# Performance work log

Hardware: AMD Instinct MI355X
Metric: run time of the kernel (lower is better)

## Reference

```python
import jax, jax.numpy as jnp
import numpy as np

N_NODES = 100_000
N_EDGES = 3_200_000
NUM_FEATURES = 128
HIDDEN = 128
NUM_CLASSES = 10
LAYERS = 3
NUM_GRAPHS = 256
EPS = 1e-5


def setup_inputs() -> dict:
    key = jax.random.key(0)
    ks = jax.random.split(key, 12)
    s = 0.05
    x = jax.random.normal(ks[0], (N_NODES, NUM_FEATURES), jnp.float32)
    edge_index = jax.random.randint(ks[1], (2, N_EDGES), 0, N_NODES, dtype=jnp.int32)
    batch = jnp.sort(jax.random.randint(ks[2], (N_NODES,), 0, NUM_GRAPHS, dtype=jnp.int32))
    lin1_W = jax.random.normal(ks[3], (NUM_FEATURES, HIDDEN), jnp.float32) * s
    lin1_b = jnp.zeros((HIDDEN,), jnp.float32)
    conv_W = jax.random.normal(ks[4], (LAYERS, HIDDEN, HIDDEN), jnp.float32) * s
    conv_b = jnp.zeros((LAYERS, HIDDEN), jnp.float32)
    mlp_W1 = jax.random.normal(ks[5], (HIDDEN, HIDDEN), jnp.float32) * s
    mlp_b1 = jnp.zeros((HIDDEN,), jnp.float32)
    mlp_W2 = jax.random.normal(ks[6], (HIDDEN, NUM_CLASSES), jnp.float32) * s
    mlp_b2 = jnp.zeros((NUM_CLASSES,), jnp.float32)
    return {
        'x': x, 'edge_index': edge_index, 'batch': batch,
        'lin1_W': lin1_W, 'lin1_b': lin1_b,
        'conv_W': conv_W, 'conv_b': conv_b,
        'mlp_W1': mlp_W1, 'mlp_b1': mlp_b1,
        'mlp_W2': mlp_W2, 'mlp_b2': mlp_b2,
    }


def reference(x, edge_index, batch, lin1_W, lin1_b, conv_W, conv_b,
              mlp_W1, mlp_b1, mlp_W2, mlp_b2):
    N = x.shape[0]
    # GCN with self-loops, all-ones edge_weight, symmetric normalization.
    loop = jnp.arange(N, dtype=edge_index.dtype)
    src = jnp.concatenate([edge_index[0], loop])
    dst = jnp.concatenate([edge_index[1], loop])
    ew = jnp.ones(src.shape[0], x.dtype)
    deg = jax.ops.segment_sum(ew, dst, num_segments=N)
    dinv = jnp.where(deg > 0, jax.lax.rsqrt(deg), 0.0)
    norm = dinv[src] * dinv[dst]  # [E+N]

    h = jax.nn.relu(x @ lin1_W + lin1_b)  # dropout is identity at eval
    for i in range(conv_W.shape[0]):
        hw = h @ conv_W[i]                       # [N,H]
        msg = hw[src] * norm[:, None]            # [E+N,H] gather
        h = jax.ops.segment_sum(msg, dst, num_segments=N) + conv_b[i]
        h = jax.nn.relu(h)
        # full-tensor LayerNorm (normalized_shape == x.size(), no affine)
        mu = jnp.mean(h)
        var = jnp.mean(jnp.square(h - mu))
        h = (h - mu) * jax.lax.rsqrt(var + EPS)

    # global mean pooling over graphs
    cnt = jax.ops.segment_sum(jnp.ones((N,), x.dtype), batch, num_segments=NUM_GRAPHS)
    pooled = jax.ops.segment_sum(h, batch, num_segments=NUM_GRAPHS) / jnp.maximum(cnt, 1.0)[:, None]

    g = jax.nn.relu(pooled @ mlp_W1 + mlp_b1)
    scores = g @ mlp_W2 + mlp_b2
    return jax.nn.log_softmax(scores, axis=-1)
```

## Files before the change

kernel.cpp:

```cpp
#include <hip/hip_runtime.h>
#include <math.h>

#define NN 100000
#define HH 128
#define NCLS 10
#define NGRAPH 256
#define EPSLN 1e-5f
#define NB 196
#define NBLK 256

typedef __attribute__((ext_vector_type(8))) short short8;
typedef __attribute__((ext_vector_type(4))) float f32x4;

static __device__ __forceinline__ unsigned short f2bf(float f){
  unsigned u = __float_as_uint(f);
  u = u + 0x7fffu + ((u >> 16) & 1u);
  return (unsigned short)(u >> 16);
}
static __device__ __forceinline__ float bf2f(unsigned short h){
  return __uint_as_float(((unsigned)h) << 16);
}

__global__ __launch_bounds__(1024) void bucket_hist(
    const int* __restrict__ dst, int E,
    int* __restrict__ gbucket, int* __restrict__ blkbase)
{
  __shared__ int lh[NB];
  int tid = threadIdx.x;
  for (int i = tid; i < NB; i += 1024) lh[i] = 0;
  __syncthreads();
  int per = (E + gridDim.x - 1) / gridDim.x;
  int s = blockIdx.x * per, e = min(E, s + per);
  for (int j = s + tid; j < e; j += 1024)
    atomicAdd(&lh[dst[j] >> 9], 1);
  __syncthreads();
  for (int i = tid; i < NB; i += 1024)
    blkbase[blockIdx.x * NB + i] = atomicAdd(&gbucket[i], lh[i]);
}

__global__ void bucket_scan(const int* __restrict__ gbucket,
                            int* __restrict__ bucket_base, int E,
                            int* __restrict__ row_ptr, int N,
                            float* __restrict__ params, float* __restrict__ stats)
{
  if (threadIdx.x == 0 && blockIdx.x == 0){
    int run = 0;
    for (int b = 0; b < NB; b++){ bucket_base[b] = run; run += gbucket[b]; }
    bucket_base[NB] = run;
    row_ptr[N] = E;
    params[0] = 0.f;
    params[1] = 1.f;
    for (int i = 0; i < 6; i++) stats[i] = 0.f;
  }
}

__global__ __launch_bounds__(1024) void bucket_scatter(
    const int* __restrict__ src, const int* __restrict__ dst, int E,
    const int* __restrict__ bucket_base, const int* __restrict__ blkbase,
    unsigned* __restrict__ ebuf)
{
  __shared__ int lcur[NB];
  int tid = threadIdx.x;
  for (int i = tid; i < NB; i += 1024)
    lcur[i] = bucket_base[i] + blkbase[blockIdx.x * NB + i];
  __syncthreads();
  int per = (E + gridDim.x - 1) / gridDim.x;
  int s = blockIdx.x * per, e = min(E, s + per);
  for (int j = s + tid; j < e; j += 1024){
    int d = dst[j];
    int p = atomicAdd(&lcur[d >> 9], 1);
    ebuf[p] = (((unsigned)(d & 511)) << 23) | (unsigned)src[j];
  }
}

__global__ __launch_bounds__(1024) void bucket_fill(
    const unsigned* __restrict__ ebuf,
    const int* __restrict__ bucket_base, int N,
    int* __restrict__ row_ptr, float* __restrict__ dinv,
    int* __restrict__ csr)
{
  __shared__ int ldeg[512];
  __shared__ int lscan[512];
  __shared__ int lcur[512];
  int b = blockIdx.x, tid = threadIdx.x;
  int node0 = b << 9;
  int nn = min(512, N - node0);
  for (int i = tid; i < 512; i += 1024) ldeg[i] = 0;
  __syncthreads();
  int s = bucket_base[b], e = bucket_base[b + 1];
  for (int j = s + tid; j < e; j += 1024)
    atomicAdd(&ldeg[ebuf[j] >> 23], 1);
  __syncthreads();
  if (tid < 512) lscan[tid] = ldeg[tid];
  __syncthreads();
  for (int off = 1; off < 512; off <<= 1){
    int v = (tid < 512 && tid >= off) ? lscan[tid - off] : 0;
    __syncthreads();
    if (tid < 512) lscan[tid] += v;
    __syncthreads();
  }
  if (tid < nn){
    int rp = s + lscan[tid] - ldeg[tid];
    row_ptr[node0 + tid] = rp;
    lcur[tid] = rp;
    dinv[node0 + tid] = rsqrtf((float)(ldeg[tid] + 1));
  }
  __syncthreads();
  for (int j = s + tid; j < e; j += 1024){
    unsigned pk = ebuf[j];
    int p = atomicAdd(&lcur[pk >> 23], 1);
    csr[p] = (int)(pk & 0x7fffffu);
  }
}

__global__ void colsum_kernel(const float* __restrict__ W, float* __restrict__ cs){
  const float* w = W + blockIdx.x*HH*HH;
  float s = 0.f;
  for (int k = 0; k < HH; k++) s += w[k*HH + threadIdx.x];
  cs[blockIdx.x*HH + threadIdx.x] = s;
}

__global__ __launch_bounds__(256) void prep_weights(
    const float* __restrict__ lin1W, const float* __restrict__ convW,
    unsigned short* __restrict__ WtAll)
{
  int m = blockIdx.x;
  const float* srcW = (m == 0) ? lin1W : convW + (size_t)(m-1)*HH*HH;
  unsigned short* dstW = WtAll + (size_t)m*HH*HH;
  for (int i = threadIdx.x; i < HH*HH; i += 256){
    int k = i >> 7, nn2 = i & 127;
    dstW[nn2*HH + k] = f2bf(srcW[i]);
  }
}

__global__ __launch_bounds__(256) void gemm_mfma(
    const float* __restrict__ A32, const unsigned short* __restrict__ A16,
    const unsigned short* __restrict__ Wt,
    const float* __restrict__ bias, const float* __restrict__ dinv,
    const float* __restrict__ params, const float* __restrict__ colsum,
    unsigned short* __restrict__ out, int n, int mode)
{
  __shared__ unsigned short As[128*128];
  __shared__ unsigned short Ws[128*128];
  int tid = threadIdx.x;
  int rb = blockIdx.x * 128;

  #pragma unroll
  for (int rep = 0; rep < 8; rep++){
    int idx = rep*256 + tid;
    int r = idx >> 4, j = idx & 15;
    uint4 v = *(const uint4*)&Wt[r*HH + j*8];
    *(uint4*)&Ws[r*128 + ((j ^ (r & 7)) << 3)] = v;
  }
  if (mode == 1){
    #pragma unroll
    for (int rep = 0; rep < 8; rep++){
      int idx = rep*256 + tid;
      int r = idx >> 4, j = idx & 15;
      int row = rb + r;
      uint4 v = make_uint4(0,0,0,0);
      if (row < n) v = *(const uint4*)&A16[(size_t)row*HH + j*8];
      *(uint4*)&As[r*128 + ((j ^ (r & 7)) << 3)] = v;
    }
  } else {
    #pragma unroll
    for (int rep = 0; rep < 16; rep++){
      int idx = rep*256 + tid;
      int r = idx >> 5, j4 = idx & 31;
      int row = rb + r;
      float4 v = make_float4(0,0,0,0);
      if (row < n) v = *(const float4*)&A32[(size_t)row*HH + j4*4];
      uint2 pk;
      pk.x = (unsigned)f2bf(v.x) | ((unsigned)f2bf(v.y) << 16);
      pk.y = (unsigned)f2bf(v.z) | ((unsigned)f2bf(v.w) << 16);
      int uidx = r*128 + ((((j4 >> 1) ^ (r & 7)) << 3)) + (j4 & 1)*4;
      *(uint2*)&As[uidx] = pk;
    }
  }
  __syncthreads();

  int l = tid & 63, w = tid >> 6;
  int lr = l & 15, lk = l >> 4;
  f32x4 acc[2][8];
  #pragma unroll
  for (int mt = 0; mt < 2; mt++)
    #pragma unroll
    for (int nt = 0; nt < 8; nt++) acc[mt][nt] = (f32x4)(0.f);

  #pragma unroll
  for (int kc = 0; kc < 4; kc++){
    short8 af[2];
    #pragma unroll
    for (int mt = 0; mt < 2; mt++){
      int row = w*32 + mt*16 + lr;
      af[mt] = *(const short8*)&As[row*128 + (((kc*4 + lk) ^ (row & 7)) << 3)];
    }
    #pragma unroll
    for (int nt = 0; nt < 8; nt++){
      int col = nt*16 + lr;
      short8 bf = *(const short8*)&Ws[col*128 + (((kc*4 + lk) ^ (col & 7)) << 3)];
      acc[0][nt] = __builtin_amdgcn_mfma_f32_16x16x32_bf16(af[0], bf, acc[0][nt], 0, 0, 0);
      acc[1][nt] = __builtin_amdgcn_mfma_f32_16x16x32_bf16(af[1], bf, acc[1][nt], 0, 0, 0);
    }
  }

  float mu = 0.f, rsig = 1.f;
  if (mode == 1){ mu = params[0]; rsig = params[1]; }
  float dvs[2][4];
  #pragma unroll
  for (int mt = 0; mt < 2; mt++)
    #pragma unroll
    for (int r = 0; r < 4; r++){
      int row = rb + w*32 + mt*16 + lk*4 + r;
      dvs[mt][r] = (mode == 1 && row < n) ? dinv[row] : 0.f;
    }
  #pragma unroll
  for (int nt = 0; nt < 8; nt++){
    int col = nt*16 + lr;
    float cs = (mode == 1) ? colsum[col] : 0.f;
    float bb = (mode == 0) ? bias[col] : 0.f;
    #pragma unroll
    for (int mt = 0; mt < 2; mt++){
      #pragma unroll
      for (int r = 0; r < 4; r++){
        int row = rb + w*32 + mt*16 + lk*4 + r;
        if (row < n){
          float a = acc[mt][nt][r];
          float vv = (mode == 0) ? fmaxf(a + bb, 0.f)
                                 : dvs[mt][r] * rsig * (a - mu*cs);
          out[(size_t)row*HH + col] = f2bf(vv);
        }
      }
    }
  }
}

__global__ __launch_bounds__(128) void aggregate(
    const unsigned short* __restrict__ hw, const int* __restrict__ row_ptr,
    const int* __restrict__ csr, const float* __restrict__ dinv,
    const float* __restrict__ bias, unsigned short* __restrict__ hout,
    float2* __restrict__ partials)
{
  int node = blockIdx.x;
  int t = threadIdx.x;
  float acc = bf2f(hw[(size_t)node*HH + t]);
  int s0 = row_ptr[node], s1 = row_ptr[node+1];
  int j = s0;
  for (; j + 16 <= s1; j += 16){
    int idx[16];
    #pragma unroll
    for (int u = 0; u < 16; u++) idx[u] = __builtin_nontemporal_load(&csr[j+u]);
    unsigned short v[16];
    #pragma unroll
    for (int u = 0; u < 16; u++) v[u] = hw[(size_t)idx[u]*HH + t];
    #pragma unroll
    for (int u = 0; u < 16; u++) acc += bf2f(v[u]);
  }
  for (; j + 4 <= s1; j += 4){
    int idx[4];
    #pragma unroll
    for (int u = 0; u < 4; u++) idx[u] = __builtin_nontemporal_load(&csr[j+u]);
    unsigned short v[4];
    #pragma unroll
    for (int u = 0; u < 4; u++) v[u] = hw[(size_t)idx[u]*HH + t];
    acc += (bf2f(v[0]) + bf2f(v[1])) + (bf2f(v[2]) + bf2f(v[3]));
  }
  for (; j < s1; j++) acc += bf2f(hw[(size_t)csr[j]*HH + t]);

  float r = fmaxf(fmaf(dinv[node], acc, bias[t]), 0.f);
  hout[(size_t)node*HH + t] = f2bf(r);

  float s = r, q = r*r;
  for (int off = 32; off > 0; off >>= 1){
    s += __shfl_xor(s, off, 64);
    q += __shfl_xor(q, off, 64);
  }
  __shared__ float sm[4];
  int wave = t >> 6, lane = t & 63;
  if (lane == 0){ sm[wave*2] = s; sm[wave*2+1] = q; }
  __syncthreads();
  if (t == 0) partials[node] = make_float2(sm[0] + sm[2], sm[1] + sm[3]);
}

__global__ __launch_bounds__(256) void finalize_part(
    const float2* __restrict__ partials, int n, float* __restrict__ stats)
{
  int tid = threadIdx.x;
  float s = 0.f, q = 0.f;
  for (int i = blockIdx.x*256 + tid; i < n; i += gridDim.x*256){
    float2 p = partials[i];
    s += p.x; q += p.y;
  }
  for (int off = 32; off > 0; off >>= 1){
    s += __shfl_xor(s, off, 64);
    q += __shfl_xor(q, off, 64);
  }
  __shared__ float ssm[4], qsm[4];
  int wave = tid >> 6, lane = tid & 63;
  if (lane == 0){ ssm[wave] = s; qsm[wave] = q; }
  __syncthreads();
  if (tid == 0){
    float S = ssm[0]+ssm[1]+ssm[2]+ssm[3];
    float Q = qsm[0]+qsm[1]+qsm[2]+qsm[3];
    atomicAdd(&stats[0], S);
    atomicAdd(&stats[1], Q);
  }
}

__global__ void finalize_fin(const float* __restrict__ stats, float* __restrict__ params){
  if (threadIdx.x == 0){
    const float inv = 1.f / ((float)NN * (float)HH);
    float mu = stats[0] * inv;
    float var = stats[1] * inv - mu*mu;
    params[0] = mu;
    params[1] = rsqrtf(var + EPSLN);
  }
}

__global__ __launch_bounds__(128) void pool_mlp(
    const unsigned short* __restrict__ h, const int* __restrict__ batch,
    const float* __restrict__ params, const float* __restrict__ W1,
    const float* __restrict__ b1, const float* __restrict__ W2,
    const float* __restrict__ b2, float* __restrict__ out, int n)
{
  __shared__ float pooled[128];
  __shared__ float gact[128];
  __shared__ float sc[16];
  __shared__ int se[2];
  int g = blockIdx.x, tid = threadIdx.x;
  if (tid < 2){
    int v = g + tid;
    int lo = 0, hi = n;
    while (lo < hi){ int mid = (lo+hi) >> 1; if (batch[mid] < v) lo = mid+1; else hi = mid; }
    se[tid] = lo;
  }
  __syncthreads();
  int start = se[0], end = se[1];
  float sum = 0.f;
  for (int v = start; v < end; v++) sum += bf2f(h[(size_t)v*HH + tid]);
  float cnt = (float)((end - start) > 0 ? (end - start) : 1);
  float mu = params[0], rs = params[1];
  pooled[tid] = rs * (sum / cnt - mu);
  __syncthreads();
  float a = b1[tid];
  for (int k = 0; k < HH; k++) a = fmaf(pooled[k], W1[k*HH + tid], a);
  gact[tid] = fmaxf(a, 0.f);
  __syncthreads();
  if (tid < NCLS){
    float s = b2[tid];
    for (int k = 0; k < HH; k++) s = fmaf(gact[k], W2[k*NCLS + tid], s);
    sc[tid] = s;
  }
  __syncthreads();
  if (tid == 0){
    float m = sc[0];
    for (int j = 1; j < NCLS; j++) m = fmaxf(m, sc[j]);
    float lse = 0.f;
    for (int j = 0; j < NCLS; j++) lse += expf(sc[j] - m);
    lse = logf(lse);
    for (int j = 0; j < NCLS; j++) out[g*NCLS + j] = sc[j] - m - lse;
  }
}

extern "C" void kernel_launch(void* const* d_in, const int* in_sizes, int n_in,
                              void* d_out, int out_size, void* d_ws, size_t ws_size,
                              hipStream_t stream)
{
  const float* x      = (const float*)d_in[0];
  const int*   ei     = (const int*)d_in[1];
  const int*   batch  = (const int*)d_in[2];
  const float* lin1_W = (const float*)d_in[3];
  const float* lin1_b = (const float*)d_in[4];
  const float* conv_W = (const float*)d_in[5];
  const float* conv_b = (const float*)d_in[6];
  const float* mlp_W1 = (const float*)d_in[7];
  const float* mlp_b1 = (const float*)d_in[8];
  const float* mlp_W2 = (const float*)d_in[9];
  const float* mlp_b2 = (const float*)d_in[10];

  const int N = in_sizes[2];
  const int E = in_sizes[1] / 2;

  char* ws = (char*)d_ws;
  size_t off = 0;
  auto alloc = [&](size_t bytes)->char*{
    char* p = ws + off; off += (bytes + 255) & ~(size_t)255; return p;
  };
  unsigned short* bufA = (unsigned short*)alloc((size_t)N*HH*2);
  unsigned short* bufB = (unsigned short*)alloc((size_t)N*HH*2);
  unsigned short* WtAll= (unsigned short*)alloc((size_t)4*HH*HH*2);
  int*      csr     = (int*)     alloc((size_t)E*4);
  unsigned* ebuf    = (unsigned*)alloc((size_t)E*4);
  int*      row_ptr = (int*)     alloc((size_t)(N+1)*4);
  float*    dinv    = (float*)   alloc((size_t)N*4);
  int*      gbucket = (int*)     alloc((size_t)NB*4);
  int*      bucket_base = (int*) alloc((size_t)(NB+1)*4);
  int*      blkbase = (int*)     alloc((size_t)NBLK*NB*4);
  float*    params  = (float*)   alloc(256);
  float*    stats   = (float*)   alloc(256);
  float*    csums   = (float*)   alloc(3*HH*4);
  float2*   partials= (float2*)  alloc((size_t)N*8);

  const int* srcp = ei;
  const int* dstp = ei + E;

  hipMemsetAsync(gbucket, 0, (size_t)NB*4, stream);
  bucket_hist<<<NBLK, 1024, 0, stream>>>(dstp, E, gbucket, blkbase);
  bucket_scan<<<1, 64, 0, stream>>>(gbucket, bucket_base, E, row_ptr, N, params, stats);
  bucket_scatter<<<NBLK, 1024, 0, stream>>>(srcp, dstp, E, bucket_base, blkbase, ebuf);
  bucket_fill<<<NB, 1024, 0, stream>>>(ebuf, bucket_base, N, row_ptr, dinv, csr);
  colsum_kernel<<<3, 128, 0, stream>>>(conv_W, csums);
  prep_weights<<<4, 256, 0, stream>>>(lin1_W, conv_W, WtAll);

  int gblocks = (N + 127) / 128;
  gemm_mfma<<<gblocks, 256, 0, stream>>>(x, nullptr, WtAll, lin1_b,
                                         nullptr, nullptr, nullptr, bufA, N, 0);
  for (int i = 0; i < 3; i++){
    gemm_mfma<<<gblocks, 256, 0, stream>>>(nullptr, bufA, WtAll + (size_t)(i+1)*HH*HH,
                                           nullptr, dinv, params + 2*i, csums + i*HH,
                                           bufB, N, 1);
    aggregate<<<N, 128, 0, stream>>>(bufB, row_ptr, csr, dinv,
                                     conv_b + i*HH, bufA, partials);
    finalize_part<<<128, 256, 0, stream>>>(partials, N, stats + 2*i);
    finalize_fin<<<1, 64, 0, stream>>>(stats + 2*i, params + 2*(i+1));
  }
  pool_mlp<<<NGRAPH, 128, 0, stream>>>(bufA, batch, params + 6,
                                       mlp_W1, mlp_b1, mlp_W2, mlp_b2,
                                       (float*)d_out, N);
}
```

Baseline: 668.4 us.

## Wave-per-node packed bf16 aggregation, replicated histograms, fused prep and LN kernels

Aggregation now assigns one wavefront per node, with each lane loading a packed pair of bf16 values as 32-bit words, and software-prefetches the next 16 CSR indices. This halves the number of gather instructions and removes the block-level shared reduction. Bucket histogram and scatter use 8 replicated shared-memory counters to cut LDS atomic contention. The scan, colsum and weight-prep kernels are merged into one launch, and the two LayerNorm finalize kernels are fused using a last-block counter. Together these reduce launch count. The changes add more blkbase traffic and a threadfence-based completion pattern.

```diff
diff --git a/kernel.cpp b/kernel.cpp
--- a/kernel.cpp
+++ b/kernel.cpp
@@ -8,6 +8,7 @@
 #define EPSLN 1e-5f
 #define NB 196
 #define NBLK 256
+#define NREP 8
 
 typedef __attribute__((ext_vector_type(8))) short short8;
 typedef __attribute__((ext_vector_type(4))) float f32x4;
@@ -25,32 +26,58 @@
     const int* __restrict__ dst, int E,
     int* __restrict__ gbucket, int* __restrict__ blkbase)
 {
-  __shared__ int lh[NB];
+  __shared__ int lh[NREP*NB];
   int tid = threadIdx.x;
-  for (int i = tid; i < NB; i += 1024) lh[i] = 0;
-  __syncthreads();
+  for (int i = tid; i < NREP*NB; i += 1024) lh[i] = 0;
+  __syncthreads();
+  int rep = (tid >> 7) & (NREP-1);
+  int* lhr = &lh[rep*NB];
   int per = (E + gridDim.x - 1) / gridDim.x;
   int s = blockIdx.x * per, e = min(E, s + per);
   for (int j = s + tid; j < e; j += 1024)
-    atomicAdd(&lh[dst[j] >> 9], 1);
-  __syncthreads();
-  for (int i = tid; i < NB; i += 1024)
-    blkbase[blockIdx.x * NB + i] = atomicAdd(&gbucket[i], lh[i]);
-}
-
-__global__ void bucket_scan(const int* __restrict__ gbucket,
-                            int* __restrict__ bucket_base, int E,
-                            int* __restrict__ row_ptr, int N,
-                            float* __restrict__ params, float* __restrict__ stats)
-{
-  if (threadIdx.x == 0 && blockIdx.x == 0){
-    int run = 0;
-    for (int b = 0; b < NB; b++){ bucket_base[b] = run; run += gbucket[b]; }
-    bucket_base[NB] = run;
-    row_ptr[N] = E;
-    params[0] = 0.f;
-    params[1] = 1.f;
-    for (int i = 0; i < 6; i++) stats[i] = 0.f;
+    atomicAdd(&lhr[dst[j] >> 9], 1);
+  __syncthreads();
+  for (int i = tid; i < NREP*NB; i += 1024){
+    int r = i / NB, bkt = i - r*NB;
+    blkbase[((size_t)blockIdx.x*NREP + r)*NB + bkt] = atomicAdd(&gbucket[bkt], lh[i]);
+  }
+}
+
+__global__ __launch_bounds__(256) void misc_prep(
+    const int* __restrict__ gbucket, int* __restrict__ bucket_base, int E,
+    int* __restrict__ row_ptr, int N,
+    float* __restrict__ params, float* __restrict__ stats, int* __restrict__ counters,
+    const float* __restrict__ lin1W, const float* __restrict__ convW,
+    unsigned short* __restrict__ WtAll, float* __restrict__ csums)
+{
+  int b = blockIdx.x;
+  if (b == 0){
+    if (threadIdx.x == 0){
+      int run = 0;
+      for (int i = 0; i < NB; i++){ bucket_base[i] = run; run += gbucket[i]; }
+      bucket_base[NB] = run;
+      row_ptr[N] = E;
+      params[0] = 0.f;
+      params[1] = 1.f;
+      for (int i = 0; i < 6; i++) stats[i] = 0.f;
+      for (int i = 0; i < 3; i++) counters[i] = 0;
+    }
+  } else if (b <= 3){
+    int m = b - 1;
+    if (threadIdx.x < HH){
+      const float* w = convW + (size_t)m*HH*HH;
+      float s = 0.f;
+      for (int k = 0; k < HH; k++) s += w[k*HH + threadIdx.x];
+      csums[m*HH + threadIdx.x] = s;
+    }
+  } else {
+    int m = b - 4;
+    const float* srcW = (m == 0) ? lin1W : convW + (size_t)(m-1)*HH*HH;
+    unsigned short* dstW = WtAll + (size_t)m*HH*HH;
+    for (int i = threadIdx.x; i < HH*HH; i += 256){
+      int k = i >> 7, nn2 = i & 127;
+      dstW[nn2*HH + k] = f2bf(srcW[i]);
+    }
   }
 }
 
@@ -59,16 +86,20 @@
     const int* __restrict__ bucket_base, const int* __restrict__ blkbase,
     unsigned* __restrict__ ebuf)
 {
-  __shared__ int lcur[NB];
+  __shared__ int lcur[NREP*NB];
   int tid = threadIdx.x;
-  for (int i = tid; i < NB; i += 1024)
-    lcur[i] = bucket_base[i] + blkbase[blockIdx.x * NB + i];
-  __syncthreads();
+  for (int i = tid; i < NREP*NB; i += 1024){
+    int r = i / NB, bkt = i - r*NB;
+    lcur[i] = bucket_base[bkt] + blkbase[((size_t)blockIdx.x*NREP + r)*NB + bkt];
+  }
+  __syncthreads();
+  int rep = (tid >> 7) & (NREP-1);
+  int* lcr = &lcur[rep*NB];
   int per = (E + gridDim.x - 1) / gridDim.x;
   int s = blockIdx.x * per, e = min(E, s + per);
   for (int j = s + tid; j < e; j += 1024){
     int d = dst[j];
-    int p = atomicAdd(&lcur[d >> 9], 1);
+    int p = atomicAdd(&lcr[d >> 9], 1);
     ebuf[p] = (((unsigned)(d & 511)) << 23) | (unsigned)src[j];
   }
 }
@@ -110,26 +141,6 @@
     unsigned pk = ebuf[j];
     int p = atomicAdd(&lcur[pk >> 23], 1);
     csr[p] = (int)(pk & 0x7fffffu);
-  }
-}
-
-__global__ void colsum_kernel(const float* __restrict__ W, float* __restrict__ cs){
-  const float* w = W + blockIdx.x*HH*HH;
-  float s = 0.f;
-  for (int k = 0; k < HH; k++) s += w[k*HH + threadIdx.x];
-  cs[blockIdx.x*HH + threadIdx.x] = s;
-}
-
-__global__ __launch_bounds__(256) void prep_weights(
-    const float* __restrict__ lin1W, const float* __restrict__ convW,
-    unsigned short* __restrict__ WtAll)
-{
-  int m = blockIdx.x;
-  const float* srcW = (m == 0) ? lin1W : convW + (size_t)(m-1)*HH*HH;
-  unsigned short* dstW = WtAll + (size_t)m*HH*HH;
-  for (int i = threadIdx.x; i < HH*HH; i += 256){
-    int k = i >> 7, nn2 = i & 127;
-    dstW[nn2*HH + k] = f2bf(srcW[i]);
   }
 }
 
@@ -235,55 +246,79 @@
   }
 }
 
-__global__ __launch_bounds__(128) void aggregate(
-    const unsigned short* __restrict__ hw, const int* __restrict__ row_ptr,
+__global__ __launch_bounds__(256) void aggregate(
+    const unsigned* __restrict__ hw, const int* __restrict__ row_ptr,
     const int* __restrict__ csr, const float* __restrict__ dinv,
-    const float* __restrict__ bias, unsigned short* __restrict__ hout,
-    float2* __restrict__ partials)
-{
-  int node = blockIdx.x;
-  int t = threadIdx.x;
-  float acc = bf2f(hw[(size_t)node*HH + t]);
+    const float* __restrict__ bias, unsigned* __restrict__ hout,
+    float2* __restrict__ partials, int n)
+{
+  int wid = __builtin_amdgcn_readfirstlane(threadIdx.x >> 6);
+  int node = blockIdx.x * 4 + wid;
+  if (node >= n) return;
+  int l = threadIdx.x & 63;
+  int selfoff = node*64 + l;
+  unsigned selfv = hw[selfoff];
+  float ax = __uint_as_float(selfv << 16);
+  float ay = __uint_as_float(selfv & 0xffff0000u);
   int s0 = row_ptr[node], s1 = row_ptr[node+1];
   int j = s0;
-  for (; j + 16 <= s1; j += 16){
-    int idx[16];
-    #pragma unroll
-    for (int u = 0; u < 16; u++) idx[u] = __builtin_nontemporal_load(&csr[j+u]);
-    unsigned short v[16];
-    #pragma unroll
-    for (int u = 0; u < 16; u++) v[u] = hw[(size_t)idx[u]*HH + t];
-    #pragma unroll
-    for (int u = 0; u < 16; u++) acc += bf2f(v[u]);
+  if (j + 16 <= s1){
+    int cur[16];
+    #pragma unroll
+    for (int u = 0; u < 16; u++) cur[u] = csr[j+u];
+    while (true){
+      unsigned v[16];
+      #pragma unroll
+      for (int u = 0; u < 16; u++) v[u] = hw[cur[u]*64 + l];
+      int jn = j + 16;
+      bool more = (jn + 16 <= s1);
+      int nxt[16];
+      if (more){
+        #pragma unroll
+        for (int u = 0; u < 16; u++) nxt[u] = csr[jn+u];
+      }
+      #pragma unroll
+      for (int u = 0; u < 16; u++){
+        ax += __uint_as_float(v[u] << 16);
+        ay += __uint_as_float(v[u] & 0xffff0000u);
+      }
+      j = jn;
+      if (!more) break;
+      #pragma unroll
+      for (int u = 0; u < 16; u++) cur[u] = nxt[u];
+    }
   }
   for (; j + 4 <= s1; j += 4){
-    int idx[4];
-    #pragma unroll
-    for (int u = 0; u < 4; u++) idx[u] = __builtin_nontemporal_load(&csr[j+u]);
-    unsigned short v[4];
-    #pragma unroll
-    for (int u = 0; u < 4; u++) v[u] = hw[(size_t)idx[u]*HH + t];
-    acc += (bf2f(v[0]) + bf2f(v[1])) + (bf2f(v[2]) + bf2f(v[3]));
-  }
-  for (; j < s1; j++) acc += bf2f(hw[(size_t)csr[j]*HH + t]);
-
-  float r = fmaxf(fmaf(dinv[node], acc, bias[t]), 0.f);
-  hout[(size_t)node*HH + t] = f2bf(r);
-
-  float s = r, q = r*r;
+    int i0 = csr[j], i1 = csr[j+1], i2 = csr[j+2], i3 = csr[j+3];
+    unsigned v0 = hw[i0*64+l], v1 = hw[i1*64+l], v2 = hw[i2*64+l], v3 = hw[i3*64+l];
+    ax += (__uint_as_float(v0<<16) + __uint_as_float(v1<<16))
+        + (__uint_as_float(v2<<16) + __uint_as_float(v3<<16));
+    ay += (__uint_as_float(v0&0xffff0000u) + __uint_as_float(v1&0xffff0000u))
+        + (__uint_as_float(v2&0xffff0000u) + __uint_as_float(v3&0xffff0000u));
+  }
+  for (; j < s1; j++){
+    unsigned v = hw[csr[j]*64 + l];
+    ax += __uint_as_float(v << 16);
+    ay += __uint_as_float(v & 0xffff0000u);
+  }
+  float dv = dinv[node];
+  float2 bb = ((const float2*)bias)[l];
+  float rx = fmaxf(fmaf(dv, ax, bb.x), 0.f);
+  float ry = fmaxf(fmaf(dv, ay, bb.y), 0.f);
+  hout[selfoff] = (unsigned)f2bf(rx) | ((unsigned)f2bf(ry) << 16);
+
+  float s = rx + ry, q = rx*rx + ry*ry;
+  #pragma unroll
   for (int off = 32; off > 0; off >>= 1){
     s += __shfl_xor(s, off, 64);
     q += __shfl_xor(q, off, 64);
   }
-  __shared__ float sm[4];
-  int wave = t >> 6, lane = t & 63;
-  if (lane == 0){ sm[wave*2] = s; sm[wave*2+1] = q; }
-  __syncthreads();
-  if (t == 0) partials[node] = make_float2(sm[0] + sm[2], sm[1] + sm[3]);
-}
-
-__global__ __launch_bounds__(256) void finalize_part(
-    const float2* __restrict__ partials, int n, float* __restrict__ stats)
+  if (l == 0) partials[node] = make_float2(s, q);
+}
+
+__global__ __launch_bounds__(256) void finalize_ln(
+    const float2* __restrict__ partials, int n, float* __restrict__ stats,
+    int* __restrict__ counter, float* __restrict__ params)
 {
   int tid = threadIdx.x;
   float s = 0.f, q = 0.f;
@@ -291,6 +326,7 @@
     float2 p = partials[i];
     s += p.x; q += p.y;
   }
+  #pragma unroll
   for (int off = 32; off > 0; off >>= 1){
     s += __shfl_xor(s, off, 64);
     q += __shfl_xor(q, off, 64);
@@ -300,20 +336,19 @@
   if (lane == 0){ ssm[wave] = s; qsm[wave] = q; }
   __syncthreads();
   if (tid == 0){
-    float S = ssm[0]+ssm[1]+ssm[2]+ssm[3];
-    float Q = qsm[0]+qsm[1]+qsm[2]+qsm[3];
-    atomicAdd(&stats[0], S);
-    atomicAdd(&stats[1], Q);
-  }
-}
-
-__global__ void finalize_fin(const float* __restrict__ stats, float* __restrict__ params){
-  if (threadIdx.x == 0){
-    const float inv = 1.f / ((float)NN * (float)HH);
-    float mu = stats[0] * inv;
-    float var = stats[1] * inv - mu*mu;
-    params[0] = mu;
-    params[1] = rsqrtf(var + EPSLN);
+    atomicAdd(&stats[0], ssm[0]+ssm[1]+ssm[2]+ssm[3]);
+    atomicAdd(&stats[1], qsm[0]+qsm[1]+qsm[2]+qsm[3]);
+    __threadfence();
+    int done = atomicAdd(counter, 1);
+    if (done == (int)gridDim.x - 1){
+      float S = atomicAdd(&stats[0], 0.f);
+      float Q = atomicAdd(&stats[1], 0.f);
+      const float inv = 1.f / ((float)NN * (float)HH);
+      float mu = S * inv;
+      float var = Q * inv - mu*mu;
+      params[0] = mu;
+      params[1] = rsqrtf(var + EPSLN);
+    }
   }
 }
 
@@ -395,9 +430,10 @@
   float*    dinv    = (float*)   alloc((size_t)N*4);
   int*      gbucket = (int*)     alloc((size_t)NB*4);
   int*      bucket_base = (int*) alloc((size_t)(NB+1)*4);
-  int*      blkbase = (int*)     alloc((size_t)NBLK*NB*4);
+  int*      blkbase = (int*)     alloc((size_t)NBLK*NREP*NB*4);
   float*    params  = (float*)   alloc(256);
   float*    stats   = (float*)   alloc(256);
+  int*      counters= (int*)     alloc(256);
   float*    csums   = (float*)   alloc(3*HH*4);
   float2*   partials= (float2*)  alloc((size_t)N*8);
 
@@ -406,11 +442,11 @@
 
   hipMemsetAsync(gbucket, 0, (size_t)NB*4, stream);
   bucket_hist<<<NBLK, 1024, 0, stream>>>(dstp, E, gbucket, blkbase);
-  bucket_scan<<<1, 64, 0, stream>>>(gbucket, bucket_base, E, row_ptr, N, params, stats);
+  misc_prep<<<8, 256, 0, stream>>>(gbucket, bucket_base, E, row_ptr, N,
+                                   params, stats, counters,
+                                   lin1_W, conv_W, WtAll, csums);
   bucket_scatter<<<NBLK, 1024, 0, stream>>>(srcp, dstp, E, bucket_base, blkbase, ebuf);
   bucket_fill<<<NB, 1024, 0, stream>>>(ebuf, bucket_base, N, row_ptr, dinv, csr);
-  colsum_kernel<<<3, 128, 0, stream>>>(conv_W, csums);
-  prep_weights<<<4, 256, 0, stream>>>(lin1_W, conv_W, WtAll);
 
   int gblocks = (N + 127) / 128;
   gemm_mfma<<<gblocks, 256, 0, stream>>>(x, nullptr, WtAll, lin1_b,
@@ -419,10 +455,10 @@
     gemm_mfma<<<gblocks, 256, 0, stream>>>(nullptr, bufA, WtAll + (size_t)(i+1)*HH*HH,
                                            nullptr, dinv, params + 2*i, csums + i*HH,
                                            bufB, N, 1);
-    aggregate<<<N, 128, 0, stream>>>(bufB, row_ptr, csr, dinv,
-                                     conv_b + i*HH, bufA, partials);
-    finalize_part<<<128, 256, 0, stream>>>(partials, N, stats + 2*i);
-    finalize_fin<<<1, 64, 0, stream>>>(stats + 2*i, params + 2*(i+1));
+    aggregate<<<(N+3)/4, 256, 0, stream>>>((const unsigned*)bufB, row_ptr, csr, dinv,
+                                           conv_b + i*HH, (unsigned*)bufA, partials, N);
+    finalize_ln<<<64, 256, 0, stream>>>(partials, N, stats + 2*i,
+                                        counters + i, params + 2*(i+1));
   }
   pool_mlp<<<NGRAPH, 128, 0, stream>>>(bufA, batch, params + 6,
                                        mlp_W1, mlp_b1, mlp_W2, mlp_b2,
```

New measurement: 679.5 us. Within noise of the previous version (+1.7%).
